# Performance work log

Hardware: AMD Instinct MI355X
Metric: run time of the kernel (lower is better)

Reference implementation:

```python
import jax, jax.numpy as jnp
import numpy as np

N, E, IN, H, C = 50000, 1600000, 128, 64, 2
# calculate_theta2(d=2): Bernstein-beta polynomial coefficients (increasing power order)
THETAS = [[3.0, -3.0, 0.75], [0.0, 3.0, -1.5], [0.0, 0.0, 0.75]]
K = 3  # polynomial order d+1


def setup_inputs() -> dict:
    key = jax.random.key(0)
    ks = jax.random.split(key, 20)
    s = 0.05
    return {
        "in_feat": jax.random.normal(ks[0], (N, IN), jnp.float32),
        "src": jax.random.randint(ks[1], (E,), 0, N, jnp.int32),
        "dst": jax.random.randint(ks[2], (E,), 0, N, jnp.int32),
        "W1": jax.random.normal(ks[3], (IN, H), jnp.float32) * s,
        "b1": jnp.zeros((H,), jnp.float32),
        "W2": jax.random.normal(ks[4], (H, H), jnp.float32) * s,
        "b2": jnp.zeros((H,), jnp.float32),
        "Wres": jax.random.normal(ks[5], (H, H), jnp.float32) * s,
        "bres": jnp.zeros((H,), jnp.float32),
        "Wattn": jax.random.normal(ks[6], (H, 1), jnp.float32) * s,
        "battn": jnp.zeros((1,), jnp.float32),
        "Wf1": jax.random.normal(ks[7], (2 * H, H), jnp.float32) * s,
        "bf1": jnp.zeros((H,), jnp.float32),
        "Wf2": jax.random.normal(ks[8], (H, 1), jnp.float32) * s,
        "bf2": jnp.zeros((1,), jnp.float32),
        "W3": jax.random.normal(ks[9], (H, H), jnp.float32) * s,
        "b3": jnp.zeros((H,), jnp.float32),
        "W4": jax.random.normal(ks[10], (H, C), jnp.float32) * s,
        "b4": jnp.zeros((C,), jnp.float32),
    }


def reference(in_feat, src, dst, W1, b1, W2, b2, Wres, bres, Wattn, battn,
              Wf1, bf1, Wf2, bf2, W3, b3, W4, b4):
    relu = jax.nn.relu
    # degree normalization: in_degrees().clamp(min=1) ** -0.5
    deg = jax.ops.segment_sum(jnp.ones((E,), in_feat.dtype), dst, num_segments=N)
    d_invsqrt = jnp.clip(deg, 1.0, None) ** -0.5  # [N]
    d_invsqrt = d_invsqrt[:, None]

    def spmm(x):  # update_all(copy_u, sum): aggregate over incoming edges
        return jax.ops.segment_sum(x[src], dst, num_segments=N)

    def laplacian(x):  # x - D^{-1/2} A D^{-1/2} x
        return x - spmm(x * d_invsqrt) * d_invsqrt

    # MLP preprocessing (dropout = identity in eval mode)
    h_pre = relu(in_feat @ W1 + b1)
    h_pre = relu(h_pre @ W2 + b2)
    res = h_pre @ Wres + bres

    # Laplacian power basis shared across branches (same math as per-branch loops)
    feats = [h_pre]
    for _ in range(K - 1):
        feats.append(laplacian(feats[-1]))

    branch_outputs = [sum(th[k] * feats[k] for k in range(K)) for th in THETAS]
    h_stack = jnp.stack(branch_outputs, axis=1)  # [N, B, H]

    # attention fusion over branches
    attn_scores = (h_stack @ Wattn + battn)[..., 0]       # [N, B]
    attn_weights = jax.nn.softmax(attn_scores, axis=1)[..., None]
    attn_fused = jnp.sum(h_stack * attn_weights, axis=1)  # [N, H]
    mean_fused = jnp.mean(h_stack, axis=1)                # [N, H]

    fusion_input = jnp.concatenate([attn_fused, mean_fused], axis=-1)  # [N, 2H]
    fusion_weight = jax.nn.sigmoid(relu(fusion_input @ Wf1 + bf1) @ Wf2 + bf2)  # [N, 1]

    fused = 0.1 * fusion_weight * attn_fused + (1.0 - fusion_weight) * mean_fused
    fused = fused + 0.8 * res
    fused = relu(fused @ W3 + b3)
    logits = fused @ W4 + b4
    return logits
```

## Files before the change

kernel.cpp:

```cpp
#include <hip/hip_runtime.h>
#include <hip/hip_fp16.h>
#include <math.h>


#define BSHIFT 7
#define BNODES 128
#define BMAX   512
#define EPT    32
#define CHUNK  (256 * EPT)
#define CAP    8192

__device__ __forceinline__ void fma4(float4& acc, float s, const float4 w) {
    acc.x += s * w.x; acc.y += s * w.y; acc.z += s * w.z; acc.w += s * w.w;
}

__device__ __forceinline__ float bcast(float v, int k) {
    return __uint_as_float(__builtin_amdgcn_readlane(__float_as_uint(v), k));
}

__device__ __forceinline__ float2 pack_half4(float x, float y, float z, float w) {
    union { __half2 h[2]; float2 f; } u;
    u.h[0] = __floats2half2_rn(x, y);
    u.h[1] = __floats2half2_rn(z, w);
    return u.f;
}

__device__ __forceinline__ void acch4(float4& a, float2 p) {
    union { float2 f; __half2 h[2]; } u; u.f = p;
    float2 lo = __half22float2(u.h[0]);
    float2 hi = __half22float2(u.h[1]);
    a.x += lo.x; a.y += lo.y; a.z += hi.x; a.w += hi.y;
}


__global__ __launch_bounds__(256) void bucket_count_k(const int* __restrict__ dst,
                                                      int* __restrict__ bucketCount,
                                                      int E, int B) {
    __shared__ int cnt[BMAX];
    for (int i = threadIdx.x; i < B; i += 256) cnt[i] = 0;
    __syncthreads();
    int base = blockIdx.x * CHUNK;
    #pragma unroll
    for (int t = 0; t < EPT; t++) {
        int e = base + t * 256 + threadIdx.x;
        if (e < E) atomicAdd(&cnt[dst[e] >> BSHIFT], 1);
    }
    __syncthreads();
    for (int i = threadIdx.x; i < B; i += 256)
        if (cnt[i] > 0) atomicAdd(&bucketCount[i], cnt[i]);
}

__global__ __launch_bounds__(64) void bucket_scan_k(const int* __restrict__ bucketCount,
                                                    int* __restrict__ bucketPtr,
                                                    int* __restrict__ bucketCursor,
                                                    int* __restrict__ rowPtr,
                                                    int B, int N, int E) {
    int lane = threadIdx.x;
    const int PT = (BMAX + 63) / 64;
    int v[PT]; int s = 0;
    #pragma unroll
    for (int t = 0; t < PT; t++) {
        int i = lane * PT + t;
        v[t] = (i < B) ? bucketCount[i] : 0;
        s += v[t];
    }
    int x = s;
    #pragma unroll
    for (int off = 1; off < 64; off <<= 1) {
        int y = __shfl_up(x, off, 64);
        if (lane >= off) x += y;
    }
    int run = x - s;
    #pragma unroll
    for (int t = 0; t < PT; t++) {
        int i = lane * PT + t;
        if (i < B) { bucketPtr[i] = run; bucketCursor[i] = run; }
        run += v[t];
    }
    if (lane == 63) bucketPtr[B] = x;
    if (lane == 0) rowPtr[N] = E;
}

__global__ __launch_bounds__(256) void bucket_scatter_k(const int* __restrict__ src,
                                                        const int* __restrict__ dst,
                                                        int* __restrict__ bucketCursor,
                                                        int* __restrict__ ebuf,
                                                        int E, int B) {
    __shared__ int cnt[BMAX];
    __shared__ int base[BMAX];
    __shared__ int cur[BMAX];
    for (int i = threadIdx.x; i < B; i += 256) { cnt[i] = 0; cur[i] = 0; }
    __syncthreads();
    int cbase = blockIdx.x * CHUNK;
    int d[EPT];
    #pragma unroll
    for (int t = 0; t < EPT; t++) {
        int e = cbase + t * 256 + threadIdx.x;
        d[t] = (e < E) ? dst[e] : -1;
        if (d[t] >= 0) atomicAdd(&cnt[d[t] >> BSHIFT], 1);
    }
    __syncthreads();
    for (int i = threadIdx.x; i < B; i += 256)
        if (cnt[i] > 0) base[i] = atomicAdd(&bucketCursor[i], cnt[i]);
    __syncthreads();
    #pragma unroll
    for (int t = 0; t < EPT; t++) {
        int e = cbase + t * 256 + threadIdx.x;
        if (d[t] >= 0) {
            int b = d[t] >> BSHIFT;
            int c = atomicAdd(&cur[b], 1);
            int pack = (src[e] & 0xFFFF) | ((d[t] & (BNODES - 1)) << 16);
            ebuf[base[b] + c] = pack;
        }
    }
}

__global__ __launch_bounds__(256) void csr_build_k(const int* __restrict__ ebuf,
                                                   const int* __restrict__ bucketPtr,
                                                   int* __restrict__ rowPtr,
                                                   float* __restrict__ dinv,
                                                   int* __restrict__ srcSorted,
                                                   int N) {
    __shared__ int deg[BNODES];
    __shared__ int rp[BNODES + 1];
    __shared__ int cur[BNODES];
    __shared__ int stage[CAP];
    int b = blockIdx.x;
    int nodeBase = b << BSHIFT;
    int nNodes = min(BNODES, N - nodeBase);
    int eBase = bucketPtr[b];
    int eCnt = bucketPtr[b + 1] - eBase;
    for (int i = threadIdx.x; i < BNODES; i += 256) deg[i] = 0;
    __syncthreads();
    for (int i = threadIdx.x; i < eCnt; i += 256)
        atomicAdd(&deg[(ebuf[eBase + i] >> 16) & (BNODES - 1)], 1);
    __syncthreads();
    if (threadIdx.x < 64) {
        int lane = threadIdx.x;
        int d0 = deg[2 * lane], d1 = deg[2 * lane + 1];
        int s = d0 + d1;
        int x = s;
        #pragma unroll
        for (int off = 1; off < 64; off <<= 1) {
            int y = __shfl_up(x, off, 64);
            if (lane >= off) x += y;
        }
        int ex = x - s;
        rp[2 * lane] = ex;
        rp[2 * lane + 1] = ex + d0;
        cur[2 * lane] = ex;
        cur[2 * lane + 1] = ex + d0;
        if (lane == 63) rp[BNODES] = x;
    }
    __syncthreads();
    for (int j = threadIdx.x; j < nNodes; j += 256) {
        rowPtr[nodeBase + j] = eBase + rp[j];
        int dg = deg[j];
        dinv[nodeBase + j] = rsqrtf((float)(dg > 1 ? dg : 1));
    }
    if (eCnt <= CAP) {
        for (int i = threadIdx.x; i < eCnt; i += 256) {
            int p = ebuf[eBase + i];
            int ld = (p >> 16) & (BNODES - 1);
            int pos = atomicAdd(&cur[ld], 1);
            stage[pos] = p & 0xFFFF;
        }
        __syncthreads();
        for (int i = threadIdx.x; i < eCnt; i += 256)
            srcSorted[eBase + i] = stage[i];
    } else {
        for (int i = threadIdx.x; i < eCnt; i += 256) {
            int p = ebuf[eBase + i];
            int ld = (p >> 16) & (BNODES - 1);
            int pos = atomicAdd(&cur[ld], 1);
            srcSorted[eBase + pos] = p & 0xFFFF;
        }
    }
}


#define D1_BLK 128
#define D1_PAD 68

__global__ __launch_bounds__(D1_BLK) void dense1_k(const float* __restrict__ Xg,
                                                   const float* __restrict__ W1,
                                                   const float* __restrict__ b1,
                                                   float* __restrict__ h1, int N) {
    __shared__ float lds[D1_BLK * D1_PAD];
    int n0 = blockIdx.x * D1_BLK;
    int n = n0 + threadIdx.x;
    bool act = (n < N);
    const float4* W = (const float4*)W1;
    const float4* B = (const float4*)b1;
    float4 acc[16];
    #pragma unroll
    for (int j = 0; j < 16; j++) acc[j] = B[j];
    if (act) {
        const float4* X = (const float4*)Xg + (size_t)n * 32;
        float4 a = X[0];
        #pragma unroll 1
        for (int kc = 0; kc < 32; kc++) {
            float4 an = a;
            if (kc + 1 < 32) an = X[kc + 1];
            const float4* wrow = W + kc * 64;
            #pragma unroll
            for (int j = 0; j < 16; j++) {
                fma4(acc[j], a.x, wrow[j]);
                fma4(acc[j], a.y, wrow[16 + j]);
                fma4(acc[j], a.z, wrow[32 + j]);
                fma4(acc[j], a.w, wrow[48 + j]);
            }
            a = an;
        }
    }
    float* myrow = &lds[threadIdx.x * D1_PAD];
    #pragma unroll
    for (int j = 0; j < 16; j++) {
        float4 v = acc[j];
        *(float4*)&myrow[4 * j] = make_float4(fmaxf(v.x, 0.f), fmaxf(v.y, 0.f),
                                              fmaxf(v.z, 0.f), fmaxf(v.w, 0.f));
    }
    __syncthreads();
    float4* o4 = (float4*)h1;
    #pragma unroll
    for (int r = 0; r < 16; r++) {
        int idx = r * D1_BLK + threadIdx.x;
        int row = idx >> 4, col = idx & 15;
        int gn = n0 + row;
        if (gn < N) o4[(size_t)gn * 16 + col] = *(float4*)&lds[row * D1_PAD + col * 4];
    }
}


#define D2_BLK 128
#define D2_PAD 68

__global__ __launch_bounds__(D2_BLK) void dense2res_k(const float* __restrict__ h1,
                                                      const float* __restrict__ W2,
                                                      const float* __restrict__ b2,
                                                      const float* __restrict__ Wres,
                                                      const float* __restrict__ bres,
                                                      const float* __restrict__ Wattn,
                                                      const float* __restrict__ dinv,
                                                      float* __restrict__ hg,
                                                      float2* __restrict__ hs2,
                                                      float* __restrict__ resg,
                                                      float* __restrict__ thv, int N) {
    __shared__ float lds[D2_BLK * D2_PAD];
    int n0 = blockIdx.x * D2_BLK;
    int n = n0 + threadIdx.x;
    bool act = (n < N);
    const float4* W = (const float4*)W2;
    const float4* B = (const float4*)b2;
    float4 acc[16];
    #pragma unroll
    for (int j = 0; j < 16; j++) acc[j] = B[j];
    if (act) {
        const float4* X = (const float4*)h1 + (size_t)n * 16;
        float4 a = X[0];
        #pragma unroll 1
        for (int kc = 0; kc < 16; kc++) {
            float4 an = a;
            if (kc + 1 < 16) an = X[kc + 1];
            const float4* wrow = W + kc * 64;
            #pragma unroll
            for (int j = 0; j < 16; j++) {
                fma4(acc[j], a.x, wrow[j]);
                fma4(acc[j], a.y, wrow[16 + j]);
                fma4(acc[j], a.z, wrow[32 + j]);
                fma4(acc[j], a.w, wrow[48 + j]);
            }
            a = an;
        }
    }
    const float4* Wa = (const float4*)Wattn;
    float th = 0.f;
    float* myrow = &lds[threadIdx.x * D2_PAD];
    #pragma unroll
    for (int j = 0; j < 16; j++) {
        float4 v = acc[j];
        v.x = fmaxf(v.x, 0.f); v.y = fmaxf(v.y, 0.f);
        v.z = fmaxf(v.z, 0.f); v.w = fmaxf(v.w, 0.f);
        acc[j] = v;
        *(float4*)&myrow[4 * j] = v;
        float4 w = Wa[j];
        th += v.x * w.x + v.y * w.y + v.z * w.z + v.w * w.w;
    }
    if (act) thv[n] = th;
    __syncthreads();
    float4* h4 = (float4*)hg;
    #pragma unroll
    for (int r = 0; r < 16; r++) {
        int idx = r * D2_BLK + threadIdx.x;
        int row = idx >> 4, col = idx & 15;
        int gn = n0 + row;
        if (gn < N) {
            float4 v = *(float4*)&lds[row * D2_PAD + col * 4];
            h4[(size_t)gn * 16 + col] = v;
            float di = dinv[gn];
            hs2[(size_t)gn * 16 + col] =
                pack_half4(v.x * di, v.y * di, v.z * di, v.w * di);
        }
    }
    const float4* WR = (const float4*)Wres;
    const float4* BR = (const float4*)bres;
    float4 acc2[16];
    #pragma unroll
    for (int j = 0; j < 16; j++) acc2[j] = BR[j];
    #pragma unroll 1
    for (int kc = 0; kc < 16; kc++) {
        float4 a2 = acc[kc];
        const float4* wrow = WR + kc * 64;
        #pragma unroll
        for (int j = 0; j < 16; j++) {
            fma4(acc2[j], a2.x, wrow[j]);
            fma4(acc2[j], a2.y, wrow[16 + j]);
            fma4(acc2[j], a2.z, wrow[32 + j]);
            fma4(acc2[j], a2.w, wrow[48 + j]);
        }
    }
    __syncthreads();
    #pragma unroll
    for (int j = 0; j < 16; j++) *(float4*)&myrow[4 * j] = acc2[j];
    __syncthreads();
    float4* r4 = (float4*)resg;
    #pragma unroll
    for (int r = 0; r < 16; r++) {
        int idx = r * D2_BLK + threadIdx.x;
        int row = idx >> 4, col = idx & 15;
        int gn = n0 + row;
        if (gn < N) r4[(size_t)gn * 16 + col] = *(float4*)&lds[row * D2_PAD + col * 4];
    }
}


__global__ __launch_bounds__(256) void spmm_k(const float2* __restrict__ xs,
                                              const int* __restrict__ srcs,
                                              const int* __restrict__ rowPtr,
                                              const float* __restrict__ dinv,
                                              const float* __restrict__ Wattn,
                                              float4* __restrict__ u,
                                              float2* __restrict__ us,
                                              float* __restrict__ tav, int N) {
    int node = (blockIdx.x * 256 + threadIdx.x) >> 6;
    if (node >= N) return;
    int lane = threadIdx.x & 63;
    int sub = lane >> 4;
    int q = lane & 15;
    int s0 = rowPtr[node], s1 = rowPtr[node + 1];
    float4 a0 = make_float4(0.f, 0.f, 0.f, 0.f);
    float4 a1 = a0, a2 = a0, a3 = a0;
    int i = s0 + sub;
    for (; i + 12 < s1; i += 16) {
        int sA = srcs[i];
        int sB = srcs[i + 4];
        int sC = srcs[i + 8];
        int sD = srcs[i + 12];
        float2 vA = xs[(size_t)sA * 16 + q];
        float2 vB = xs[(size_t)sB * 16 + q];
        float2 vC = xs[(size_t)sC * 16 + q];
        float2 vD = xs[(size_t)sD * 16 + q];
        acch4(a0, vA); acch4(a1, vB); acch4(a2, vC); acch4(a3, vD);
    }
    for (; i + 4 < s1; i += 8) {
        int sA = srcs[i];
        int sB = srcs[i + 4];
        float2 vA = xs[(size_t)sA * 16 + q];
        float2 vB = xs[(size_t)sB * 16 + q];
        acch4(a0, vA); acch4(a1, vB);
    }
    if (i < s1) {
        float2 vA = xs[(size_t)srcs[i] * 16 + q];
        acch4(a0, vA);
    }
    a0.x += a1.x + a2.x + a3.x;
    a0.y += a1.y + a2.y + a3.y;
    a0.z += a1.z + a2.z + a3.z;
    a0.w += a1.w + a2.w + a3.w;
    #pragma unroll
    for (int m = 16; m < 64; m <<= 1) {
        a0.x += __shfl_xor(a0.x, m, 64);
        a0.y += __shfl_xor(a0.y, m, 64);
        a0.z += __shfl_xor(a0.z, m, 64);
        a0.w += __shfl_xor(a0.w, m, 64);
    }
    if (sub == 0) {
        float di = dinv[node];
        float4 r = make_float4(a0.x * di, a0.y * di, a0.z * di, a0.w * di);
        u[(size_t)node * 16 + q] = r;
        us[(size_t)node * 16 + q] =
            pack_half4(r.x * di, r.y * di, r.z * di, r.w * di);
        float4 w = ((const float4*)Wattn)[q];
        float p = r.x * w.x + r.y * w.y + r.z * w.z + r.w * w.w;
        #pragma unroll
        for (int m = 1; m < 16; m <<= 1) p += __shfl_xor(p, m, 64);
        if (lane == 0) tav[node] = p;
    }
}


#define TL_PAD 68

__global__ __launch_bounds__(256) void tail_k(const float2* __restrict__ u1s,
                                              const int* __restrict__ srcs,
                                              const int* __restrict__ rowPtr,
                                              const float* __restrict__ dinv,
                                              const float* __restrict__ hg,
                                              const float* __restrict__ u1g,
                                              const float* __restrict__ resg,
                                              const float* __restrict__ thv,
                                              const float* __restrict__ tav,
                                              const float* __restrict__ Wattn,
                                              const float* __restrict__ battn,
                                              const float* __restrict__ Wf1,
                                              const float* __restrict__ bf1,
                                              const float* __restrict__ Wf2,
                                              const float* __restrict__ bf2,
                                              const float* __restrict__ W3,
                                              const float* __restrict__ b3,
                                              const float* __restrict__ W4,
                                              const float* __restrict__ b4,
                                              float2* __restrict__ out, int N) {
    __shared__ float lds[4 * TL_PAD];
    int w = threadIdx.x >> 6;
    int lane = threadIdx.x & 63;
    int node = blockIdx.x * 4 + w;
    if (node >= N) return;
    int sub = lane >> 4, q = lane & 15;
    {
        int s0 = rowPtr[node], s1 = rowPtr[node + 1];
        float4 a0 = make_float4(0.f, 0.f, 0.f, 0.f);
        float4 a1 = a0, a2 = a0, a3 = a0;
        int i = s0 + sub;
        for (; i + 12 < s1; i += 16) {
            int sA = srcs[i];
            int sB = srcs[i + 4];
            int sC = srcs[i + 8];
            int sD = srcs[i + 12];
            float2 vA = u1s[(size_t)sA * 16 + q];
            float2 vB = u1s[(size_t)sB * 16 + q];
            float2 vC = u1s[(size_t)sC * 16 + q];
            float2 vD = u1s[(size_t)sD * 16 + q];
            acch4(a0, vA); acch4(a1, vB); acch4(a2, vC); acch4(a3, vD);
        }
        for (; i + 4 < s1; i += 8) {
            int sA = srcs[i];
            int sB = srcs[i + 4];
            float2 vA = u1s[(size_t)sA * 16 + q];
            float2 vB = u1s[(size_t)sB * 16 + q];
            acch4(a0, vA); acch4(a1, vB);
        }
        if (i < s1) {
            float2 vA = u1s[(size_t)srcs[i] * 16 + q];
            acch4(a0, vA);
        }
        a0.x += a1.x + a2.x + a3.x;
        a0.y += a1.y + a2.y + a3.y;
        a0.z += a1.z + a2.z + a3.z;
        a0.w += a1.w + a2.w + a3.w;
        #pragma unroll
        for (int m = 16; m < 64; m <<= 1) {
            a0.x += __shfl_xor(a0.x, m, 64);
            a0.y += __shfl_xor(a0.y, m, 64);
            a0.z += __shfl_xor(a0.z, m, 64);
            a0.w += __shfl_xor(a0.w, m, 64);
        }
        if (sub == 0) {
            float di = dinv[node];
            *(float4*)&lds[w * TL_PAD + q * 4] =
                make_float4(a0.x * di, a0.y * di, a0.z * di, a0.w * di);
        }
    }
    float u2j = lds[w * TL_PAD + lane];
    float hj = hg[(size_t)node * 64 + lane];
    float u1j = u1g[(size_t)node * 64 + lane];
    float resj = resg[(size_t)node * 64 + lane];
    float tb = u2j * Wattn[lane];
    #pragma unroll
    for (int m = 1; m < 64; m <<= 1) tb += __shfl_xor(tb, m, 64);
    float th = thv[node], ta = tav[node], ba = battn[0];
    float s0 = 0.75f * th + 1.5f * ta + 0.75f * tb + ba;
    float s1 = 1.5f * th - 1.5f * tb + ba;
    float s2 = 0.75f * th - 1.5f * ta + 0.75f * tb + ba;
    float mx = fmaxf(s0, fmaxf(s1, s2));
    float e0 = expf(s0 - mx), e1 = expf(s1 - mx), e2 = expf(s2 - mx);
    float inv = 1.f / (e0 + e1 + e2);
    float w0 = e0 * inv, w1 = e1 * inv, w2 = e2 * inv;
    float ca = 0.75f * w0 + 1.5f * w1 + 0.75f * w2;
    float cb = 1.5f * (w0 - w2);
    float cc = 0.75f * w0 - 1.5f * w1 + 0.75f * w2;
    float afj = ca * hj + cb * u1j + cc * u2j;
    float t = bf1[lane];
    #pragma unroll 4
    for (int k = 0; k < 64; k++) {
        float afk = bcast(afj, k);
        float hk = bcast(hj, k);
        t += afk * Wf1[k * 64 + lane] + hk * Wf1[(64 + k) * 64 + lane];
    }
    t = fmaxf(t, 0.f);
    float fwacc = t * Wf2[lane];
    #pragma unroll
    for (int m = 1; m < 64; m <<= 1) fwacc += __shfl_xor(fwacc, m, 64);
    float fw = 1.f / (1.f + expf(-(fwacc + bf2[0])));
    float fj = 0.1f * fw * afj + (1.f - fw) * hj + 0.8f * resj;
    float g = b3[lane];
    #pragma unroll 4
    for (int k = 0; k < 64; k++) {
        float fk = bcast(fj, k);
        g += fk * W3[k * 64 + lane];
    }
    g = fmaxf(g, 0.f);
    float2 w4 = ((const float2*)W4)[lane];
    float l0 = g * w4.x, l1 = g * w4.y;
    #pragma unroll
    for (int m = 1; m < 64; m <<= 1) {
        l0 += __shfl_xor(l0, m, 64);
        l1 += __shfl_xor(l1, m, 64);
    }
    if (lane == 0) out[node] = make_float2(l0 + b4[0], l1 + b4[1]);
}


extern "C" void kernel_launch(void* const* d_in, const int* in_sizes, int n_in,
                              void* d_out, int out_size, void* d_ws, size_t ws_size,
                              hipStream_t stream) {
    const float* in_feat = (const float*)d_in[0];
    const int*   src     = (const int*)d_in[1];
    const int*   dst     = (const int*)d_in[2];
    const float* W1   = (const float*)d_in[3];
    const float* b1   = (const float*)d_in[4];
    const float* W2   = (const float*)d_in[5];
    const float* b2   = (const float*)d_in[6];
    const float* Wres = (const float*)d_in[7];
    const float* bres = (const float*)d_in[8];
    const float* Wattn = (const float*)d_in[9];
    const float* battn = (const float*)d_in[10];
    const float* Wf1  = (const float*)d_in[11];
    const float* bf1  = (const float*)d_in[12];
    const float* Wf2  = (const float*)d_in[13];
    const float* bf2  = (const float*)d_in[14];
    const float* W3   = (const float*)d_in[15];
    const float* b3   = (const float*)d_in[16];
    const float* W4   = (const float*)d_in[17];
    const float* b4   = (const float*)d_in[18];

    const int N = in_sizes[0] / 128;
    const int E = in_sizes[1];
    const int B = (N + BNODES - 1) >> BSHIFT;

    char* p = (char*)d_ws;
    auto take = [&](size_t bytes) -> char* {
        char* r = p;
        p += (bytes + 255) & ~(size_t)255;
        return r;
    };
    int*   bucketCount  = (int*)take((size_t)(B + 1) * 4);
    int*   bucketPtr    = (int*)take((size_t)(B + 1) * 4);
    int*   bucketCursor = (int*)take((size_t)(B + 1) * 4);
    int*   rowPtr       = (int*)take((size_t)(N + 1) * 4);
    float* dinv         = (float*)take((size_t)N * 4);
    int*   srcSorted    = (int*)take((size_t)E * 4);
    float* thv          = (float*)take((size_t)N * 4);
    float* tav          = (float*)take((size_t)N * 4);
    float* h1  = (float*)take((size_t)N * 256);
    float* h   = (float*)take((size_t)N * 256);
    float* hs  = (float*)take((size_t)N * 128);
    float* res = (float*)take((size_t)N * 256);
    float* u1  = (float*)take((size_t)N * 256);
    float* u1s = (float*)take((size_t)N * 128);
    int*   ebuf = (int*)h1;

    int eb = (E + CHUNK - 1) / CHUNK;
    int d1b = (N + D1_BLK - 1) / D1_BLK;
    int d2b = (N + D2_BLK - 1) / D2_BLK;
    int spb = (N * 64 + 255) / 256;
    int tlb = (N + 3) / 4;

    hipMemsetAsync(bucketCount, 0, (size_t)B * 4, stream);
    bucket_count_k<<<eb, 256, 0, stream>>>(dst, bucketCount, E, B);
    bucket_scan_k<<<1, 64, 0, stream>>>(bucketCount, bucketPtr, bucketCursor,
                                        rowPtr, B, N, E);
    bucket_scatter_k<<<eb, 256, 0, stream>>>(src, dst, bucketCursor, ebuf, E, B);
    csr_build_k<<<B, 256, 0, stream>>>(ebuf, bucketPtr, rowPtr, dinv, srcSorted, N);

    dense1_k<<<d1b, D1_BLK, 0, stream>>>(in_feat, W1, b1, h1, N);
    dense2res_k<<<d2b, D2_BLK, 0, stream>>>(h1, W2, b2, Wres, bres, Wattn, dinv,
                                            h, (float2*)hs, res, thv, N);

    spmm_k<<<spb, 256, 0, stream>>>((const float2*)hs, srcSorted, rowPtr, dinv,
                                    Wattn, (float4*)u1, (float2*)u1s, tav, N);

    tail_k<<<tlb, 256, 0, stream>>>((const float2*)u1s, srcSorted, rowPtr, dinv,
                                    h, u1, res, thv, tav, Wattn, battn,
                                    Wf1, bf1, Wf2, bf2, W3, b3, W4, b4,
                                    (float2*)d_out, N);
}
```

Before: 393.8 us.

## Precompute per-basis GEMV projections and split tail into spmm2 plus thread-per-node final

Uses linearity of the fusion and W3 layers: projects h, u1 and res through Wf1 and W3 ahead of time (in dense2res and a new dense_u1 kernel). A thread-per-node final kernel then combines these projections with per-node attention coefficients and only computes the u2 projections itself. This replaces the wave-per-node tail, which did serial readlane-broadcast GEMVs, with register-blocked per-thread GEMVs. In exchange it writes and reads several extra N×64 float buffers and adds two kernel launches, so the tail becomes more memory-bound.

```diff
diff --git a/kernel.cpp b/kernel.cpp
--- a/kernel.cpp
+++ b/kernel.cpp
@@ -12,10 +12,6 @@
 
 __device__ __forceinline__ void fma4(float4& acc, float s, const float4 w) {
     acc.x += s * w.x; acc.y += s * w.y; acc.z += s * w.z; acc.w += s * w.w;
-}
-
-__device__ __forceinline__ float bcast(float v, int k) {
-    return __uint_as_float(__builtin_amdgcn_readlane(__float_as_uint(v), k));
 }
 
 __device__ __forceinline__ float2 pack_half4(float x, float y, float z, float w) {
@@ -235,21 +231,65 @@
 #define D2_BLK 128
 #define D2_PAD 68
 
+#define COOP_WRITE_F32(OUT) do {                                               \
+    __syncthreads();                                                           \
+    float* myrow_ = &lds[threadIdx.x * D2_PAD];                                \
+    _Pragma("unroll")                                                          \
+    for (int j_ = 0; j_ < 16; j_++) *(float4*)&myrow_[4 * j_] = acc2[j_];      \
+    __syncthreads();                                                           \
+    float4* o4_ = (float4*)(OUT);                                              \
+    _Pragma("unroll")                                                          \
+    for (int r_ = 0; r_ < 16; r_++) {                                          \
+        int idx_ = r_ * D2_BLK + threadIdx.x;                                  \
+        int row_ = idx_ >> 4, col_ = idx_ & 15;                                \
+        int gn_ = n0 + row_;                                                   \
+        if (gn_ < N)                                                           \
+            o4_[(size_t)gn_ * 16 + col_] =                                     \
+                *(float4*)&lds[row_ * D2_PAD + col_ * 4];                      \
+    }                                                                          \
+} while (0)
+
+#define GEMV16(SRC4, WB4, SX) do {                                             \
+    _Pragma("unroll 1")                                                        \
+    for (int kc_ = 0; kc_ < 16; kc_++) {                                       \
+        float4 a_ = (SRC4)[kc_];                                               \
+        a_.x *= (SX); a_.y *= (SX); a_.z *= (SX); a_.w *= (SX);                \
+        const float4* wr_ = (WB4) + kc_ * 64;                                  \
+        _Pragma("unroll")                                                      \
+        for (int j_ = 0; j_ < 16; j_++) {                                      \
+            fma4(acc2[j_], a_.x, wr_[j_]);                                     \
+            fma4(acc2[j_], a_.y, wr_[16 + j_]);                                \
+            fma4(acc2[j_], a_.z, wr_[32 + j_]);                                \
+            fma4(acc2[j_], a_.w, wr_[48 + j_]);                                \
+        }                                                                      \
+    }                                                                          \
+} while (0)
+
+
 __global__ __launch_bounds__(D2_BLK) void dense2res_k(const float* __restrict__ h1,
                                                       const float* __restrict__ W2,
                                                       const float* __restrict__ b2,
                                                       const float* __restrict__ Wres,
                                                       const float* __restrict__ bres,
                                                       const float* __restrict__ Wattn,
+                                                      const float* __restrict__ Wf1,
+                                                      const float* __restrict__ bf1,
+                                                      const float* __restrict__ W3,
+                                                      const float* __restrict__ b3,
                                                       const float* __restrict__ dinv,
                                                       float* __restrict__ hg,
                                                       float2* __restrict__ hs2,
                                                       float* __restrict__ resg,
+                                                      float* __restrict__ Ph,
+                                                      float* __restrict__ QhB,
+                                                      float* __restrict__ Rh,
+                                                      float* __restrict__ Rresb,
                                                       float* __restrict__ thv, int N) {
     __shared__ float lds[D2_BLK * D2_PAD];
     int n0 = blockIdx.x * D2_BLK;
     int n = n0 + threadIdx.x;
     bool act = (n < N);
+    int nn = act ? n : n0;
     const float4* W = (const float4*)W2;
     const float4* B = (const float4*)b2;
     float4 acc[16];
@@ -281,7 +321,6 @@
         float4 v = acc[j];
         v.x = fmaxf(v.x, 0.f); v.y = fmaxf(v.y, 0.f);
         v.z = fmaxf(v.z, 0.f); v.w = fmaxf(v.w, 0.f);
-        acc[j] = v;
         *(float4*)&myrow[4 * j] = v;
         float4 w = Wa[j];
         th += v.x * w.x + v.y * w.y + v.z * w.z + v.w * w.w;
@@ -302,34 +341,70 @@
                 pack_half4(v.x * di, v.y * di, v.z * di, v.w * di);
         }
     }
-    const float4* WR = (const float4*)Wres;
-    const float4* BR = (const float4*)bres;
+    __syncthreads();
+    const float4* hr = (const float4*)hg + (size_t)nn * 16;
     float4 acc2[16];
-    #pragma unroll
-    for (int j = 0; j < 16; j++) acc2[j] = BR[j];
-    #pragma unroll 1
-    for (int kc = 0; kc < 16; kc++) {
-        float4 a2 = acc[kc];
-        const float4* wrow = WR + kc * 64;
-        #pragma unroll
-        for (int j = 0; j < 16; j++) {
-            fma4(acc2[j], a2.x, wrow[j]);
-            fma4(acc2[j], a2.y, wrow[16 + j]);
-            fma4(acc2[j], a2.z, wrow[32 + j]);
-            fma4(acc2[j], a2.w, wrow[48 + j]);
-        }
-    }
-    __syncthreads();
-    #pragma unroll
-    for (int j = 0; j < 16; j++) *(float4*)&myrow[4 * j] = acc2[j];
-    __syncthreads();
-    float4* r4 = (float4*)resg;
-    #pragma unroll
-    for (int r = 0; r < 16; r++) {
-        int idx = r * D2_BLK + threadIdx.x;
-        int row = idx >> 4, col = idx & 15;
-        int gn = n0 + row;
-        if (gn < N) r4[(size_t)gn * 16 + col] = *(float4*)&lds[row * D2_PAD + col * 4];
+    const float4* Wf14 = (const float4*)Wf1;
+    const float4* W34 = (const float4*)W3;
+    {
+        const float4* BB = (const float4*)bres;
+        #pragma unroll
+        for (int j = 0; j < 16; j++) acc2[j] = BB[j];
+        GEMV16(hr, (const float4*)Wres, 1.0f);
+        COOP_WRITE_F32(resg);
+    }
+    {
+        #pragma unroll
+        for (int j = 0; j < 16; j++) acc2[j] = make_float4(0.f, 0.f, 0.f, 0.f);
+        GEMV16(hr, Wf14, 1.0f);
+        COOP_WRITE_F32(Ph);
+    }
+    {
+        const float4* BB = (const float4*)bf1;
+        #pragma unroll
+        for (int j = 0; j < 16; j++) acc2[j] = BB[j];
+        GEMV16(hr, Wf14 + 1024, 1.0f);
+        COOP_WRITE_F32(QhB);
+    }
+    {
+        #pragma unroll
+        for (int j = 0; j < 16; j++) acc2[j] = make_float4(0.f, 0.f, 0.f, 0.f);
+        GEMV16(hr, W34, 1.0f);
+        COOP_WRITE_F32(Rh);
+    }
+    {
+        const float4* rr = (const float4*)resg + (size_t)nn * 16;
+        const float4* BB = (const float4*)b3;
+        #pragma unroll
+        for (int j = 0; j < 16; j++) acc2[j] = BB[j];
+        GEMV16(rr, W34, 0.8f);
+        COOP_WRITE_F32(Rresb);
+    }
+}
+
+
+__global__ __launch_bounds__(D2_BLK) void dense_u1_k(const float* __restrict__ u1,
+                                                     const float* __restrict__ Wf1,
+                                                     const float* __restrict__ W3,
+                                                     float* __restrict__ Pu1,
+                                                     float* __restrict__ Ru1, int N) {
+    __shared__ float lds[D2_BLK * D2_PAD];
+    int n0 = blockIdx.x * D2_BLK;
+    int n = n0 + threadIdx.x;
+    int nn = (n < N) ? n : n0;
+    const float4* ur = (const float4*)u1 + (size_t)nn * 16;
+    float4 acc2[16];
+    {
+        #pragma unroll
+        for (int j = 0; j < 16; j++) acc2[j] = make_float4(0.f, 0.f, 0.f, 0.f);
+        GEMV16(ur, (const float4*)Wf1, 1.0f);
+        COOP_WRITE_F32(Pu1);
+    }
+    {
+        #pragma unroll
+        for (int j = 0; j < 16; j++) acc2[j] = make_float4(0.f, 0.f, 0.f, 0.f);
+        GEMV16(ur, (const float4*)W3, 1.0f);
+        COOP_WRITE_F32(Ru1);
     }
 }
 
@@ -399,86 +474,89 @@
 }
 
 
-#define TL_PAD 68
-
-__global__ __launch_bounds__(256) void tail_k(const float2* __restrict__ u1s,
-                                              const int* __restrict__ srcs,
-                                              const int* __restrict__ rowPtr,
-                                              const float* __restrict__ dinv,
-                                              const float* __restrict__ hg,
-                                              const float* __restrict__ u1g,
-                                              const float* __restrict__ resg,
-                                              const float* __restrict__ thv,
-                                              const float* __restrict__ tav,
-                                              const float* __restrict__ Wattn,
-                                              const float* __restrict__ battn,
-                                              const float* __restrict__ Wf1,
-                                              const float* __restrict__ bf1,
-                                              const float* __restrict__ Wf2,
-                                              const float* __restrict__ bf2,
-                                              const float* __restrict__ W3,
-                                              const float* __restrict__ b3,
-                                              const float* __restrict__ W4,
-                                              const float* __restrict__ b4,
-                                              float2* __restrict__ out, int N) {
-    __shared__ float lds[4 * TL_PAD];
-    int w = threadIdx.x >> 6;
+__global__ __launch_bounds__(256) void spmm2_k(const float2* __restrict__ u1s,
+                                               const int* __restrict__ srcs,
+                                               const int* __restrict__ rowPtr,
+                                               const float* __restrict__ dinv,
+                                               const float* __restrict__ Wattn,
+                                               float2* __restrict__ u2s,
+                                               float* __restrict__ tbv, int N) {
+    int node = (blockIdx.x * 256 + threadIdx.x) >> 6;
+    if (node >= N) return;
     int lane = threadIdx.x & 63;
-    int node = blockIdx.x * 4 + w;
-    if (node >= N) return;
-    int sub = lane >> 4, q = lane & 15;
-    {
-        int s0 = rowPtr[node], s1 = rowPtr[node + 1];
-        float4 a0 = make_float4(0.f, 0.f, 0.f, 0.f);
-        float4 a1 = a0, a2 = a0, a3 = a0;
-        int i = s0 + sub;
-        for (; i + 12 < s1; i += 16) {
-            int sA = srcs[i];
-            int sB = srcs[i + 4];
-            int sC = srcs[i + 8];
-            int sD = srcs[i + 12];
-            float2 vA = u1s[(size_t)sA * 16 + q];
-            float2 vB = u1s[(size_t)sB * 16 + q];
-            float2 vC = u1s[(size_t)sC * 16 + q];
-            float2 vD = u1s[(size_t)sD * 16 + q];
-            acch4(a0, vA); acch4(a1, vB); acch4(a2, vC); acch4(a3, vD);
-        }
-        for (; i + 4 < s1; i += 8) {
-            int sA = srcs[i];
-            int sB = srcs[i + 4];
-            float2 vA = u1s[(size_t)sA * 16 + q];
-            float2 vB = u1s[(size_t)sB * 16 + q];
-            acch4(a0, vA); acch4(a1, vB);
-        }
-        if (i < s1) {
-            float2 vA = u1s[(size_t)srcs[i] * 16 + q];
-            acch4(a0, vA);
-        }
-        a0.x += a1.x + a2.x + a3.x;
-        a0.y += a1.y + a2.y + a3.y;
-        a0.z += a1.z + a2.z + a3.z;
-        a0.w += a1.w + a2.w + a3.w;
-        #pragma unroll
-        for (int m = 16; m < 64; m <<= 1) {
-            a0.x += __shfl_xor(a0.x, m, 64);
-            a0.y += __shfl_xor(a0.y, m, 64);
-            a0.z += __shfl_xor(a0.z, m, 64);
-            a0.w += __shfl_xor(a0.w, m, 64);
-        }
-        if (sub == 0) {
-            float di = dinv[node];
-            *(float4*)&lds[w * TL_PAD + q * 4] =
-                make_float4(a0.x * di, a0.y * di, a0.z * di, a0.w * di);
-        }
-    }
-    float u2j = lds[w * TL_PAD + lane];
-    float hj = hg[(size_t)node * 64 + lane];
-    float u1j = u1g[(size_t)node * 64 + lane];
-    float resj = resg[(size_t)node * 64 + lane];
-    float tb = u2j * Wattn[lane];
-    #pragma unroll
-    for (int m = 1; m < 64; m <<= 1) tb += __shfl_xor(tb, m, 64);
-    float th = thv[node], ta = tav[node], ba = battn[0];
+    int sub = lane >> 4;
+    int q = lane & 15;
+    int s0 = rowPtr[node], s1 = rowPtr[node + 1];
+    float4 a0 = make_float4(0.f, 0.f, 0.f, 0.f);
+    float4 a1 = a0, a2 = a0, a3 = a0;
+    int i = s0 + sub;
+    for (; i + 12 < s1; i += 16) {
+        int sA = srcs[i];
+        int sB = srcs[i + 4];
+        int sC = srcs[i + 8];
+        int sD = srcs[i + 12];
+        float2 vA = u1s[(size_t)sA * 16 + q];
+        float2 vB = u1s[(size_t)sB * 16 + q];
+        float2 vC = u1s[(size_t)sC * 16 + q];
+        float2 vD = u1s[(size_t)sD * 16 + q];
+        acch4(a0, vA); acch4(a1, vB); acch4(a2, vC); acch4(a3, vD);
+    }
+    for (; i + 4 < s1; i += 8) {
+        int sA = srcs[i];
+        int sB = srcs[i + 4];
+        float2 vA = u1s[(size_t)sA * 16 + q];
+        float2 vB = u1s[(size_t)sB * 16 + q];
+        acch4(a0, vA); acch4(a1, vB);
+    }
+    if (i < s1) {
+        float2 vA = u1s[(size_t)srcs[i] * 16 + q];
+        acch4(a0, vA);
+    }
+    a0.x += a1.x + a2.x + a3.x;
+    a0.y += a1.y + a2.y + a3.y;
+    a0.z += a1.z + a2.z + a3.z;
+    a0.w += a1.w + a2.w + a3.w;
+    #pragma unroll
+    for (int m = 16; m < 64; m <<= 1) {
+        a0.x += __shfl_xor(a0.x, m, 64);
+        a0.y += __shfl_xor(a0.y, m, 64);
+        a0.z += __shfl_xor(a0.z, m, 64);
+        a0.w += __shfl_xor(a0.w, m, 64);
+    }
+    if (sub == 0) {
+        float di = dinv[node];
+        float4 r = make_float4(a0.x * di, a0.y * di, a0.z * di, a0.w * di);
+        u2s[(size_t)node * 16 + q] = pack_half4(r.x, r.y, r.z, r.w);
+        float4 w = ((const float4*)Wattn)[q];
+        float p = r.x * w.x + r.y * w.y + r.z * w.z + r.w * w.w;
+        #pragma unroll
+        for (int m = 1; m < 16; m <<= 1) p += __shfl_xor(p, m, 64);
+        if (lane == 0) tbv[node] = p;
+    }
+}
+
+
+__global__ __launch_bounds__(256) void final_k(const float4* __restrict__ u2s4,
+                                               const float* __restrict__ thv,
+                                               const float* __restrict__ tav,
+                                               const float* __restrict__ tbv,
+                                               const float* __restrict__ battn,
+                                               const float* __restrict__ Ph,
+                                               const float* __restrict__ Pu1,
+                                               const float* __restrict__ QhB,
+                                               const float* __restrict__ Rh,
+                                               const float* __restrict__ Ru1,
+                                               const float* __restrict__ Rresb,
+                                               const float* __restrict__ Wf1,
+                                               const float* __restrict__ W3,
+                                               const float* __restrict__ Wf2,
+                                               const float* __restrict__ bf2,
+                                               const float* __restrict__ W4,
+                                               const float* __restrict__ b4,
+                                               float2* __restrict__ out, int N) {
+    int n = blockIdx.x * 256 + threadIdx.x;
+    if (n >= N) return;
+    float th = thv[n], ta = tav[n], tb = tbv[n], ba = battn[0];
     float s0 = 0.75f * th + 1.5f * ta + 0.75f * tb + ba;
     float s1 = 1.5f * th - 1.5f * tb + ba;
     float s2 = 0.75f * th - 1.5f * ta + 0.75f * tb + ba;
@@ -489,35 +567,90 @@
     float ca = 0.75f * w0 + 1.5f * w1 + 0.75f * w2;
     float cb = 1.5f * (w0 - w2);
     float cc = 0.75f * w0 - 1.5f * w1 + 0.75f * w2;
-    float afj = ca * hj + cb * u1j + cc * u2j;
-    float t = bf1[lane];
-    #pragma unroll 4
-    for (int k = 0; k < 64; k++) {
-        float afk = bcast(afj, k);
-        float hk = bcast(hj, k);
-        t += afk * Wf1[k * 64 + lane] + hk * Wf1[(64 + k) * 64 + lane];
-    }
-    t = fmaxf(t, 0.f);
-    float fwacc = t * Wf2[lane];
-    #pragma unroll
-    for (int m = 1; m < 64; m <<= 1) fwacc += __shfl_xor(fwacc, m, 64);
+
+    const float4* u2r = u2s4 + (size_t)n * 8;
+    float4 acc[16];
+
+    {
+        const float4* WT = (const float4*)Wf1;
+        #pragma unroll
+        for (int j = 0; j < 16; j++) acc[j] = make_float4(0.f, 0.f, 0.f, 0.f);
+        #pragma unroll 1
+        for (int t = 0; t < 8; t++) {
+            union { float4 f; __half2 h[4]; } u; u.f = u2r[t];
+            float a[8];
+            #pragma unroll
+            for (int e = 0; e < 4; e++) {
+                float2 v = __half22float2(u.h[e]);
+                a[2 * e] = v.x; a[2 * e + 1] = v.y;
+            }
+            const float4* wr = WT + (t * 8) * 16;
+            #pragma unroll
+            for (int e = 0; e < 8; e++) {
+                #pragma unroll
+                for (int j = 0; j < 16; j++) fma4(acc[j], a[e], wr[e * 16 + j]);
+            }
+        }
+    }
+    const float4* Ph4 = (const float4*)Ph + (size_t)n * 16;
+    const float4* Pu14 = (const float4*)Pu1 + (size_t)n * 16;
+    const float4* Qh4 = (const float4*)QhB + (size_t)n * 16;
+    const float4* Wf24 = (const float4*)Wf2;
+    float fwacc = 0.f;
+    #pragma unroll
+    for (int j = 0; j < 16; j++) {
+        float4 ph = Ph4[j], pu = Pu14[j], qh = Qh4[j], pw = acc[j];
+        float4 tt;
+        tt.x = fmaxf(ca * ph.x + cb * pu.x + cc * pw.x + qh.x, 0.f);
+        tt.y = fmaxf(ca * ph.y + cb * pu.y + cc * pw.y + qh.y, 0.f);
+        tt.z = fmaxf(ca * ph.z + cb * pu.z + cc * pw.z + qh.z, 0.f);
+        tt.w = fmaxf(ca * ph.w + cb * pu.w + cc * pw.w + qh.w, 0.f);
+        float4 wf = Wf24[j];
+        fwacc += tt.x * wf.x + tt.y * wf.y + tt.z * wf.z + tt.w * wf.w;
+    }
     float fw = 1.f / (1.f + expf(-(fwacc + bf2[0])));
-    float fj = 0.1f * fw * afj + (1.f - fw) * hj + 0.8f * resj;
-    float g = b3[lane];
-    #pragma unroll 4
-    for (int k = 0; k < 64; k++) {
-        float fk = bcast(fj, k);
-        g += fk * W3[k * 64 + lane];
-    }
-    g = fmaxf(g, 0.f);
-    float2 w4 = ((const float2*)W4)[lane];
-    float l0 = g * w4.x, l1 = g * w4.y;
-    #pragma unroll
-    for (int m = 1; m < 64; m <<= 1) {
-        l0 += __shfl_xor(l0, m, 64);
-        l1 += __shfl_xor(l1, m, 64);
-    }
-    if (lane == 0) out[node] = make_float2(l0 + b4[0], l1 + b4[1]);
+
+    {
+        const float4* WT = (const float4*)W3;
+        #pragma unroll
+        for (int j = 0; j < 16; j++) acc[j] = make_float4(0.f, 0.f, 0.f, 0.f);
+        #pragma unroll 1
+        for (int t = 0; t < 8; t++) {
+            union { float4 f; __half2 h[4]; } u; u.f = u2r[t];
+            float a[8];
+            #pragma unroll
+            for (int e = 0; e < 4; e++) {
+                float2 v = __half22float2(u.h[e]);
+                a[2 * e] = v.x; a[2 * e + 1] = v.y;
+            }
+            const float4* wr = WT + (t * 8) * 16;
+            #pragma unroll
+            for (int e = 0; e < 8; e++) {
+                #pragma unroll
+                for (int j = 0; j < 16; j++) fma4(acc[j], a[e], wr[e * 16 + j]);
+            }
+        }
+    }
+    const float4* Rh4 = (const float4*)Rh + (size_t)n * 16;
+    const float4* Ru14 = (const float4*)Ru1 + (size_t)n * 16;
+    const float4* Rb4 = (const float4*)Rresb + (size_t)n * 16;
+    const float4* W44 = (const float4*)W4;
+    float sa = 0.1f * fw;
+    float sh = 1.f - fw;
+    float l0 = 0.f, l1 = 0.f;
+    #pragma unroll
+    for (int j = 0; j < 16; j++) {
+        float4 rh = Rh4[j], ru = Ru14[j], rb = Rb4[j], rw = acc[j];
+        float4 g;
+        g.x = fmaxf(sa * (ca * rh.x + cb * ru.x + cc * rw.x) + sh * rh.x + rb.x, 0.f);
+        g.y = fmaxf(sa * (ca * rh.y + cb * ru.y + cc * rw.y) + sh * rh.y + rb.y, 0.f);
+        g.z = fmaxf(sa * (ca * rh.z + cb * ru.z + cc * rw.z) + sh * rh.z + rb.z, 0.f);
+        g.w = fmaxf(sa * (ca * rh.w + cb * ru.w + cc * rw.w) + sh * rh.w + rb.w, 0.f);
+        float4 wa = W44[j * 2], wb = W44[j * 2 + 1];
+        l0 += g.x * wa.x + g.y * wa.z + g.z * wb.x + g.w * wb.z;
+        l1 += g.x * wa.y + g.y * wa.w + g.z * wb.y + g.w * wb.w;
+    }
+    out[n] = make_float2(l0 + b4[0], l1 + b4[1]);
 }
 
 
@@ -562,19 +695,27 @@
     int*   srcSorted    = (int*)take((size_t)E * 4);
     float* thv          = (float*)take((size_t)N * 4);
     float* tav          = (float*)take((size_t)N * 4);
-    float* h1  = (float*)take((size_t)N * 256);
-    float* h   = (float*)take((size_t)N * 256);
-    float* hs  = (float*)take((size_t)N * 128);
-    float* res = (float*)take((size_t)N * 256);
-    float* u1  = (float*)take((size_t)N * 256);
-    float* u1s = (float*)take((size_t)N * 128);
+    float* tbv          = (float*)take((size_t)N * 4);
+    float* h1   = (float*)take((size_t)N * 256);
+    float* h    = (float*)take((size_t)N * 256);
+    float* hs   = (float*)take((size_t)N * 128);
+    float* res  = (float*)take((size_t)N * 256);
+    float* u1   = (float*)take((size_t)N * 256);
+    float* u1s  = (float*)take((size_t)N * 128);
+    float* u2s  = (float*)take((size_t)N * 128);
+    float* QhB  = (float*)take((size_t)N * 256);
+    float* Rh   = (float*)take((size_t)N * 256);
+    float* Rresb= (float*)take((size_t)N * 256);
     int*   ebuf = (int*)h1;
+    float* Ph   = h1;
+    float* Pu1  = res;
+    float* Ru1  = h;
 
     int eb = (E + CHUNK - 1) / CHUNK;
     int d1b = (N + D1_BLK - 1) / D1_BLK;
     int d2b = (N + D2_BLK - 1) / D2_BLK;
     int spb = (N * 64 + 255) / 256;
-    int tlb = (N + 3) / 4;
+    int fnb = (N + 255) / 256;
 
     hipMemsetAsync(bucketCount, 0, (size_t)B * 4, stream);
     bucket_count_k<<<eb, 256, 0, stream>>>(dst, bucketCount, E, B);
@@ -584,14 +725,21 @@
     csr_build_k<<<B, 256, 0, stream>>>(ebuf, bucketPtr, rowPtr, dinv, srcSorted, N);
 
     dense1_k<<<d1b, D1_BLK, 0, stream>>>(in_feat, W1, b1, h1, N);
-    dense2res_k<<<d2b, D2_BLK, 0, stream>>>(h1, W2, b2, Wres, bres, Wattn, dinv,
-                                            h, (float2*)hs, res, thv, N);
+    dense2res_k<<<d2b, D2_BLK, 0, stream>>>(h1, W2, b2, Wres, bres, Wattn,
+                                            Wf1, bf1, W3, b3, dinv,
+                                            h, (float2*)hs, res,
+                                            Ph, QhB, Rh, Rresb, thv, N);
 
     spmm_k<<<spb, 256, 0, stream>>>((const float2*)hs, srcSorted, rowPtr, dinv,
                                     Wattn, (float4*)u1, (float2*)u1s, tav, N);
 
-    tail_k<<<tlb, 256, 0, stream>>>((const float2*)u1s, srcSorted, rowPtr, dinv,
-                                    h, u1, res, thv, tav, Wattn, battn,
-                                    Wf1, bf1, Wf2, bf2, W3, b3, W4, b4,
-                                    (float2*)d_out, N);
-}
+    dense_u1_k<<<d2b, D2_BLK, 0, stream>>>(u1, Wf1, W3, Pu1, Ru1, N);
+
+    spmm2_k<<<spb, 256, 0, stream>>>((const float2*)u1s, srcSorted, rowPtr, dinv,
+                                     Wattn, (float2*)u2s, tbv, N);
+
+    final_k<<<fnb, 256, 0, stream>>>((const float4*)u2s, thv, tav, tbv, battn,
+                                     Ph, Pu1, QhB, Rh, Ru1, Rresb,
+                                     Wf1, W3, Wf2, bf2, W4, b4,
+                                     (float2*)d_out, N);
+}
```

New measurement: 488.2 us. 1.24x slower.
